# Kernel optimization log

Hardware: AMD Instinct MI355X
Metric: run time of the kernel (lower is better)

The kernel has to match this reference:

```python
import jax, jax.numpy as jnp
import numpy as np

H_DIM = 64      # input_dim of edge_aggregation (== h_dim)
HID = 128       # hidden_size of each per-edge-type agg MLP
T = 5           # edge_types for non-nba dataset
B, E, N = 64, 1024, 512


def setup_inputs() -> dict:
    key = jax.random.key(0)
    ks = jax.random.split(key, 8)
    edge_distribution = jax.random.uniform(ks[0], (B, E, T), dtype=jnp.float32)
    H = jax.random.uniform(ks[1], (B, E, N), dtype=jnp.float32)
    ori = jax.random.normal(ks[2], (B, N, H_DIM), dtype=jnp.float32)
    s1 = 1.0 / np.sqrt(H_DIM)
    s2 = 1.0 / np.sqrt(HID)
    # stacked per-edge-type MLP params: Linear(64->128) -> ReLU -> Linear(128->64)
    W1 = jax.random.uniform(ks[3], (T, H_DIM, HID), minval=-s1, maxval=s1, dtype=jnp.float32)
    b1 = jax.random.uniform(ks[4], (T, HID), minval=-s1, maxval=s1, dtype=jnp.float32)
    W2 = jax.random.uniform(ks[5], (T, HID, H_DIM), minval=-s2, maxval=s2, dtype=jnp.float32)
    b2 = jax.random.uniform(ks[6], (T, H_DIM), minval=-s2, maxval=s2, dtype=jnp.float32)
    return {"edge_distribution": edge_distribution, "H": H, "ori": ori,
            "W1": W1, "b1": b1, "W2": W2, "b2": b2}


def reference(edge_distribution, H, ori, W1, b1, W2, b2):
    # incidence gather: hyperedge features [B, E, D]
    edges = jnp.matmul(H, ori)
    # per-edge-type 2-layer MLP, vectorized over the T edge types
    h = jax.nn.relu(jnp.einsum('bed,tdh->bteh', edges, W1) + b1[None, :, None, :])
    per_type = jnp.einsum('bteh,thd->bted', h, W2) + b2[None, :, None, :]
    # mixture-weighted sum over edge types -> [B, E, D]
    edge_feature = jnp.einsum('bet,bted->bed', edge_distribution, per_type)
    # scatter back through H^T and concat with original node features
    node_agg = jnp.einsum('ben,bed->bnd', H, edge_feature)  # H^T @ edge_feature
    node_feature = jnp.concatenate((node_agg, ori), axis=-1)  # [B, N, 2D]
    return node_feature
```

## Files before the change

kernel.cpp:

```cpp
#include <hip/hip_runtime.h>

#define B_   64
#define E_   1024
#define N_   512
#define D_   64
#define HID_ 128
#define T_   5

typedef __bf16 bf16x8 __attribute__((ext_vector_type(8)));
typedef float f32x4 __attribute__((ext_vector_type(4)));

__device__ __forceinline__ unsigned short f2bu(float f) {
    union { float f; unsigned int u; } v; v.f = f;
    unsigned int r = (v.u + 0x7fffu + ((v.u >> 16) & 1u)) >> 16;
    return (unsigned short)r;
}

__device__ __forceinline__ unsigned int pack2(float lo, float hi) {
    union { __bf16 b[2]; unsigned int u; } v;
    v.b[0] = (__bf16)lo; v.b[1] = (__bf16)hi;
    return v.u;
}

__device__ __forceinline__ uint4 cvt8(float4 a, float4 b) {
    union { __bf16 h[8]; uint4 u; } v;
    v.h[0] = (__bf16)a.x; v.h[1] = (__bf16)a.y; v.h[2] = (__bf16)a.z; v.h[3] = (__bf16)a.w;
    v.h[4] = (__bf16)b.x; v.h[5] = (__bf16)b.y; v.h[6] = (__bf16)b.z; v.h[7] = (__bf16)b.w;
    return v.u;
}

#define MFMA16(a, b, c) __builtin_amdgcn_mfma_f32_16x16x32_bf16((a), (b), (c), 0, 0, 0)

__global__ __launch_bounds__(256) void k_prep_w(const float* __restrict__ W1,
                                                const float* __restrict__ W2,
                                                unsigned short* __restrict__ W1T,
                                                unsigned short* __restrict__ W2T) {
    int idx = blockIdx.x * 256 + threadIdx.x;
    if (idx < T_ * HID_ * D_) {
        int t = idx / (HID_ * D_), rem = idx % (HID_ * D_);
        int h = rem / D_, d = rem % D_;
        W1T[idx] = f2bu(W1[(t * D_ + d) * HID_ + h]);
    } else {
        int j = idx - T_ * HID_ * D_;
        int t = j / (D_ * HID_), rem = j % (D_ * HID_);
        int d = rem / HID_, h = rem % HID_;
        W2T[j] = f2bu(W2[(t * HID_ + h) * D_ + d]);
    }
}

__global__ __launch_bounds__(256) void k_ori_prep(const float* __restrict__ ori,
                                                  float* __restrict__ out,
                                                  unsigned short* __restrict__ oriT) {
    int b = blockIdx.y, n0 = blockIdx.x * 64;
    __shared__ float tl[64 * 65];
    int tid = threadIdx.x;
    int dl = tid & 63;
    #pragma unroll 4
    for (int p = 0; p < 16; ++p) {
        int nn = p * 4 + (tid >> 6);
        float v = ori[(size_t)(b * N_ + n0 + nn) * D_ + dl];
        out[(size_t)(b * N_ + n0 + nn) * 128 + 64 + dl] = v;
        tl[dl * 65 + nn] = v;
    }
    __syncthreads();
    #pragma unroll 4
    for (int p = 0; p < 16; ++p) {
        int dd = p * 4 + (tid >> 6);
        oriT[(size_t)(b * D_ + dd) * N_ + n0 + dl] = f2bu(tl[dd * 65 + dl]);
    }
}

__global__ __launch_bounds__(256, 3) void k_edge_mlp(const float* __restrict__ H,
                                                     const unsigned short* __restrict__ oriT,
                                                     const float* __restrict__ ed,
                                                     const float* __restrict__ b1,
                                                     const float* __restrict__ b2,
                                                     const unsigned short* __restrict__ W1T,
                                                     const unsigned short* __restrict__ W2T,
                                                     unsigned short* __restrict__ efT) {
    int bid = blockIdx.x;
    int bx = (bid & 7) * 128 + (bid >> 3);
    int b = bx >> 4, e0 = (bx & 15) * 64;
    __shared__ __align__(16) unsigned short X[18432];
    __shared__ __align__(16) unsigned short a_sh[64 * 72];
    __shared__ float wd_sh[320];
    __shared__ float b1_sh[640];
    __shared__ float b2_sh[320];
    int tid = threadIdx.x, w = tid >> 6, l = tid & 63, q = l >> 4, c = l & 15;
    int rs = tid >> 3, sgs = tid & 7;

    uint4 w1r[4], w2r[4];
    #pragma unroll
    for (int p = 0; p < 4; ++p) {
        int u2 = p * 256 + tid;
        w1r[p] = *(const uint4*)&W1T[(u2 >> 3) * D_ + (u2 & 7) * 8];
        w2r[p] = *(const uint4*)&W2T[(u2 >> 4) * HID_ + (u2 & 15) * 8];
    }

    for (int u = tid; u < 320; u += 256) wd_sh[u] = ed[((size_t)b * E_ + e0) * T_ + u];
    for (int u = tid; u < 640; u += 256) b1_sh[u] = b1[u];
    for (int u = tid; u < 320; u += 256) b2_sh[u] = b2[u];

    const f32x4 zero = {0.f, 0.f, 0.f, 0.f};

    f32x4 acc1[4];
    #pragma unroll
    for (int fn = 0; fn < 4; ++fn) acc1[fn] = zero;

    const float* Hb = &H[((size_t)b * E_ + e0) * N_];
    const unsigned short* Ob = &oriT[(size_t)b * D_ * N_];

    float4 f00, f01, f10, f11;
    uint4 ob0, ob1;
    {
        const float* s0 = Hb + (size_t)rs * N_ + sgs * 8;
        const float* s1 = Hb + (size_t)(rs + 32) * N_ + sgs * 8;
        f00 = *(const float4*)&s0[0]; f01 = *(const float4*)&s0[4];
        f10 = *(const float4*)&s1[0]; f11 = *(const float4*)&s1[4];
        ob0 = *(const uint4*)&Ob[(size_t)rs * N_ + sgs * 8];
        ob1 = *(const uint4*)&Ob[(size_t)(rs + 32) * N_ + sgs * 8];
    }
    {
        unsigned short* aA = X;
        unsigned short* bB = X + 4608;
        *(uint4*)&aA[rs * 72 + sgs * 8] = cvt8(f00, f01);
        *(uint4*)&aA[(rs + 32) * 72 + sgs * 8] = cvt8(f10, f11);
        *(uint4*)&bB[rs * 72 + sgs * 8] = ob0;
        *(uint4*)&bB[(rs + 32) * 72 + sgs * 8] = ob1;
    }
    __syncthreads();

    for (int ks = 0; ks < 8; ++ks) {
        if (ks < 7) {
            int k0 = (ks + 1) * 64;
            const float* s0 = Hb + (size_t)rs * N_ + k0 + sgs * 8;
            const float* s1 = Hb + (size_t)(rs + 32) * N_ + k0 + sgs * 8;
            f00 = *(const float4*)&s0[0]; f01 = *(const float4*)&s0[4];
            f10 = *(const float4*)&s1[0]; f11 = *(const float4*)&s1[4];
            ob0 = *(const uint4*)&Ob[(size_t)rs * N_ + k0 + sgs * 8];
            ob1 = *(const uint4*)&Ob[(size_t)(rs + 32) * N_ + k0 + sgs * 8];
        }
        const unsigned short* aA = X + (ks & 1) * 9216;
        const unsigned short* bB = aA + 4608;
        #pragma unroll
        for (int hh = 0; hh < 2; ++hh) {
            bf16x8 a0 = *(const bf16x8*)&aA[(w * 16 + c) * 72 + hh * 32 + q * 8];
            #pragma unroll
            for (int fn = 0; fn < 4; ++fn) {
                bf16x8 bb = *(const bf16x8*)&bB[(fn * 16 + c) * 72 + hh * 32 + q * 8];
                acc1[fn] = MFMA16(a0, bb, acc1[fn]);
            }
        }
        if (ks < 7) {
            unsigned short* aN = X + ((ks & 1) ^ 1) * 9216;
            unsigned short* bN = aN + 4608;
            *(uint4*)&aN[rs * 72 + sgs * 8] = cvt8(f00, f01);
            *(uint4*)&aN[(rs + 32) * 72 + sgs * 8] = cvt8(f10, f11);
            *(uint4*)&bN[rs * 72 + sgs * 8] = ob0;
            *(uint4*)&bN[(rs + 32) * 72 + sgs * 8] = ob1;
            __syncthreads();
        }
    }
    #pragma unroll
    for (int fn = 0; fn < 4; ++fn)
        #pragma unroll
        for (int i = 0; i < 4; ++i)
            a_sh[(w * 16 + q * 4 + i) * 72 + fn * 16 + c] = f2bu(acc1[fn][i]);

    f32x4 y[4];
    #pragma unroll
    for (int fn = 0; fn < 4; ++fn) y[fn] = zero;

    unsigned short* w_sh = X;
    unsigned short* h_sh = X + 9216;

    for (int t = 0; t < T_; ++t) {
        __syncthreads();
        #pragma unroll
        for (int p = 0; p < 4; ++p) {
            int u2 = p * 256 + tid;
            *(uint4*)&w_sh[(u2 >> 3) * 72 + (u2 & 7) * 8] = w1r[p];
        }
        if (t < 4) {
            #pragma unroll
            for (int p = 0; p < 4; ++p) {
                int u2 = p * 256 + tid;
                w1r[p] = *(const uint4*)&W1T[((t + 1) * HID_ + (u2 >> 3)) * D_ + (u2 & 7) * 8];
            }
        }
        __syncthreads();
        f32x4 hc[8];
        #pragma unroll
        for (int fn = 0; fn < 8; ++fn) hc[fn] = zero;
        #pragma unroll
        for (int ks = 0; ks < 2; ++ks) {
            bf16x8 a = *(const bf16x8*)&a_sh[(w * 16 + c) * 72 + ks * 32 + q * 8];
            #pragma unroll
            for (int fn = 0; fn < 8; ++fn) {
                bf16x8 bb = *(const bf16x8*)&w_sh[(fn * 16 + c) * 72 + ks * 32 + q * 8];
                hc[fn] = MFMA16(a, bb, hc[fn]);
            }
        }
        float wv[4];
        #pragma unroll
        for (int i = 0; i < 4; ++i) wv[i] = wd_sh[(w * 16 + q * 4 + i) * T_ + t];
        #pragma unroll
        for (int fn = 0; fn < 8; ++fn) {
            float b1v = b1_sh[t * HID_ + fn * 16 + c];
            #pragma unroll
            for (int i = 0; i < 4; ++i) {
                float v = hc[fn][i] + b1v;
                v = fmaxf(v, 0.0f) * wv[i];
                h_sh[(w * 16 + q * 4 + i) * 136 + fn * 16 + c] = f2bu(v);
            }
        }
        __syncthreads();
        #pragma unroll
        for (int p = 0; p < 4; ++p) {
            int u2 = p * 256 + tid;
            *(uint4*)&w_sh[(u2 >> 4) * 136 + (u2 & 15) * 8] = w2r[p];
        }
        if (t < 4) {
            #pragma unroll
            for (int p = 0; p < 4; ++p) {
                int u2 = p * 256 + tid;
                w2r[p] = *(const uint4*)&W2T[((t + 1) * D_ + (u2 >> 4)) * HID_ + (u2 & 15) * 8];
            }
        }
        __syncthreads();
        #pragma unroll
        for (int ks = 0; ks < 4; ++ks) {
            bf16x8 a = *(const bf16x8*)&h_sh[(w * 16 + c) * 136 + ks * 32 + q * 8];
            #pragma unroll
            for (int fn = 0; fn < 4; ++fn) {
                bf16x8 bb = *(const bf16x8*)&w_sh[(fn * 16 + c) * 136 + ks * 32 + q * 8];
                y[fn] = MFMA16(a, bb, y[fn]);
            }
        }
    }
    #pragma unroll
    for (int fn = 0; fn < 4; ++fn) {
        int d = fn * 16 + c;
        ushort4 o;
        #pragma unroll
        for (int i = 0; i < 4; ++i) {
            int r = w * 16 + q * 4 + i;
            float s = y[fn][i];
            #pragma unroll
            for (int t = 0; t < T_; ++t) s += wd_sh[r * T_ + t] * b2_sh[t * D_ + d];
            ((unsigned short*)&o)[i] = f2bu(s);
        }
        *(ushort4*)&efT[((size_t)b * D_ + d) * E_ + e0 + w * 16 + q * 4] = o;
    }
}

__global__ __launch_bounds__(256) void k_gemm_out(const float* __restrict__ H,
                                                  const unsigned short* __restrict__ efT,
                                                  float* __restrict__ out) {
    int bid = blockIdx.x;
    int swz = (bid & 7) * 64 + (bid >> 3);
    int b = swz >> 3, n0 = (swz & 7) * 64;
    __shared__ __align__(16) unsigned short aA[2][64 * 72];
    __shared__ unsigned int bB32[2][64 * 33];
    int tid = threadIdx.x, w = tid >> 6, l = tid & 63, q = l >> 4, c = l & 15;
    int r2 = tid >> 3, cg = tid & 7;
    const f32x4 zero = {0.f, 0.f, 0.f, 0.f};
    f32x4 acc[4];
    #pragma unroll
    for (int fm = 0; fm < 4; ++fm) acc[fm] = zero;

    const unsigned short* Ab = &efT[(size_t)b * D_ * E_];
    const float* Hb = &H[(size_t)b * E_ * N_ + n0];

    uint4 ar0, ar1;
    float4 f0, f1, g0, g1;
    {
        ar0 = *(const uint4*)&Ab[(size_t)r2 * E_ + cg * 8];
        ar1 = *(const uint4*)&Ab[(size_t)(r2 + 32) * E_ + cg * 8];
        const float* s0 = Hb + (size_t)(2 * r2) * N_ + cg * 8;
        const float* s1 = s0 + N_;
        f0 = *(const float4*)&s0[0]; f1 = *(const float4*)&s0[4];
        g0 = *(const float4*)&s1[0]; g1 = *(const float4*)&s1[4];
    }
    {
        *(uint4*)&aA[0][r2 * 72 + cg * 8] = ar0;
        *(uint4*)&aA[0][(r2 + 32) * 72 + cg * 8] = ar1;
        float r0a[8] = {f0.x, f0.y, f0.z, f0.w, f1.x, f1.y, f1.z, f1.w};
        float r1a[8] = {g0.x, g0.y, g0.z, g0.w, g1.x, g1.y, g1.z, g1.w};
        #pragma unroll
        for (int j = 0; j < 8; ++j)
            bB32[0][(cg * 8 + j) * 33 + r2] = pack2(r0a[j], r1a[j]);
    }
    __syncthreads();

    for (int ks = 0; ks < 16; ++ks) {
        if (ks < 15) {
            int k0 = (ks + 1) * 64;
            ar0 = *(const uint4*)&Ab[(size_t)r2 * E_ + k0 + cg * 8];
            ar1 = *(const uint4*)&Ab[(size_t)(r2 + 32) * E_ + k0 + cg * 8];
            const float* s0 = Hb + (size_t)(k0 + 2 * r2) * N_ + cg * 8;
            const float* s1 = s0 + N_;
            f0 = *(const float4*)&s0[0]; f1 = *(const float4*)&s0[4];
            g0 = *(const float4*)&s1[0]; g1 = *(const float4*)&s1[4];
        }
        int cur = ks & 1;
        #pragma unroll
        for (int hh = 0; hh < 2; ++hh) {
            union { unsigned int u[4]; bf16x8 v; } bb;
            #pragma unroll
            for (int i = 0; i < 4; ++i)
                bb.u[i] = bB32[cur][(w * 16 + c) * 33 + hh * 16 + q * 4 + i];
            #pragma unroll
            for (int fm = 0; fm < 4; ++fm) {
                bf16x8 afr = *(const bf16x8*)&aA[cur][(fm * 16 + c) * 72 + hh * 32 + q * 8];
                acc[fm] = MFMA16(afr, bb.v, acc[fm]);
            }
        }
        if (ks < 15) {
            int nxt = cur ^ 1;
            *(uint4*)&aA[nxt][r2 * 72 + cg * 8] = ar0;
            *(uint4*)&aA[nxt][(r2 + 32) * 72 + cg * 8] = ar1;
            float r0a[8] = {f0.x, f0.y, f0.z, f0.w, f1.x, f1.y, f1.z, f1.w};
            float r1a[8] = {g0.x, g0.y, g0.z, g0.w, g1.x, g1.y, g1.z, g1.w};
            #pragma unroll
            for (int j = 0; j < 8; ++j)
                bB32[nxt][(cg * 8 + j) * 33 + r2] = pack2(r0a[j], r1a[j]);
            __syncthreads();
        }
    }
    #pragma unroll
    for (int fm = 0; fm < 4; ++fm) {
        *(f32x4*)&out[((size_t)b * N_ + n0 + w * 16 + c) * 128 + fm * 16 + q * 4] = acc[fm];
    }
}

extern "C" void kernel_launch(void* const* d_in, const int* in_sizes, int n_in,
                              void* d_out, int out_size, void* d_ws, size_t ws_size,
                              hipStream_t stream) {
    const float* ed  = (const float*)d_in[0];
    const float* H   = (const float*)d_in[1];
    const float* ori = (const float*)d_in[2];
    const float* W1  = (const float*)d_in[3];
    const float* b1  = (const float*)d_in[4];
    const float* W2  = (const float*)d_in[5];
    const float* b2  = (const float*)d_in[6];
    float* out = (float*)d_out;

    char* ws = (char*)d_ws;
    unsigned short* oriT = (unsigned short*)ws; ws += (size_t)B_ * D_ * N_ * 2;
    unsigned short* W1T  = (unsigned short*)ws; ws += (size_t)T_ * HID_ * D_ * 2;
    unsigned short* W2T  = (unsigned short*)ws; ws += (size_t)T_ * D_ * HID_ * 2;
    unsigned short* efT  = (unsigned short*)ws; ws += (size_t)B_ * D_ * E_ * 2;

    hipLaunchKernelGGL(k_prep_w, dim3(320), dim3(256), 0, stream, W1, W2, W1T, W2T);
    hipLaunchKernelGGL(k_ori_prep, dim3(8, 64), dim3(256), 0, stream, ori, out, oriT);
    hipLaunchKernelGGL(k_edge_mlp, dim3(1024), dim3(256), 0, stream,
                       H, oriT, ed, b1, b2, W1T, W2T, efT);
    hipLaunchKernelGGL(k_gemm_out, dim3(512), dim3(256), 0, stream, H, efT, out);
}
```

Baseline: 307.7 us.

## Swizzle LDS tiles, read MLP weights from global, drop per-type barriers

Replaces the padded LDS rows (stride 72/136) with XOR-swizzled unpadded rows, which shrinks shared memory. The MLP weight fragments are now read straight from global/L2 instead of being staged through LDS with register prefetch, and the A fragments are hoisted into registers. Each wave keeps its own private h tile, so the per-type __syncthreads calls go away. The occupancy hint (3 blocks) and the blockIdx remapping are also removed. The cost is repeated global loads of the weights on every MFMA and a possible change in L2 locality for H.

After: 336.6 us. 1.09x slower.

```diff
diff --git a/kernel.cpp b/kernel.cpp
--- a/kernel.cpp
+++ b/kernel.cpp
@@ -70,32 +70,23 @@
     }
 }
 
-__global__ __launch_bounds__(256, 3) void k_edge_mlp(const float* __restrict__ H,
-                                                     const unsigned short* __restrict__ oriT,
-                                                     const float* __restrict__ ed,
-                                                     const float* __restrict__ b1,
-                                                     const float* __restrict__ b2,
-                                                     const unsigned short* __restrict__ W1T,
-                                                     const unsigned short* __restrict__ W2T,
-                                                     unsigned short* __restrict__ efT) {
-    int bid = blockIdx.x;
-    int bx = (bid & 7) * 128 + (bid >> 3);
+__global__ __launch_bounds__(256) void k_edge_mlp(const float* __restrict__ H,
+                                                  const unsigned short* __restrict__ oriT,
+                                                  const float* __restrict__ ed,
+                                                  const float* __restrict__ b1,
+                                                  const float* __restrict__ b2,
+                                                  const unsigned short* __restrict__ W1T,
+                                                  const unsigned short* __restrict__ W2T,
+                                                  unsigned short* __restrict__ efT) {
+    int bx = blockIdx.x;
     int b = bx >> 4, e0 = (bx & 15) * 64;
-    __shared__ __align__(16) unsigned short X[18432];
-    __shared__ __align__(16) unsigned short a_sh[64 * 72];
+    __shared__ __align__(16) unsigned short X[16384];
     __shared__ float wd_sh[320];
     __shared__ float b1_sh[640];
     __shared__ float b2_sh[320];
     int tid = threadIdx.x, w = tid >> 6, l = tid & 63, q = l >> 4, c = l & 15;
     int rs = tid >> 3, sgs = tid & 7;
-
-    uint4 w1r[4], w2r[4];
-    #pragma unroll
-    for (int p = 0; p < 4; ++p) {
-        int u2 = p * 256 + tid;
-        w1r[p] = *(const uint4*)&W1T[(u2 >> 3) * D_ + (u2 & 7) * 8];
-        w2r[p] = *(const uint4*)&W2T[(u2 >> 4) * HID_ + (u2 & 15) * 8];
-    }
+    int swsl = (sgs ^ (rs & 7)) * 8;
 
     for (int u = tid; u < 320; u += 256) wd_sh[u] = ed[((size_t)b * E_ + e0) * T_ + u];
     for (int u = tid; u < 640; u += 256) b1_sh[u] = b1[u];
@@ -122,11 +113,11 @@
     }
     {
         unsigned short* aA = X;
-        unsigned short* bB = X + 4608;
-        *(uint4*)&aA[rs * 72 + sgs * 8] = cvt8(f00, f01);
-        *(uint4*)&aA[(rs + 32) * 72 + sgs * 8] = cvt8(f10, f11);
-        *(uint4*)&bB[rs * 72 + sgs * 8] = ob0;
-        *(uint4*)&bB[(rs + 32) * 72 + sgs * 8] = ob1;
+        unsigned short* bB = X + 4096;
+        *(uint4*)&aA[rs * 64 + swsl] = cvt8(f00, f01);
+        *(uint4*)&aA[(rs + 32) * 64 + swsl] = cvt8(f10, f11);
+        *(uint4*)&bB[rs * 64 + swsl] = ob0;
+        *(uint4*)&bB[(rs + 32) * 64 + swsl] = ob1;
     }
     __syncthreads();
 
@@ -140,65 +131,62 @@
             ob0 = *(const uint4*)&Ob[(size_t)rs * N_ + k0 + sgs * 8];
             ob1 = *(const uint4*)&Ob[(size_t)(rs + 32) * N_ + k0 + sgs * 8];
         }
-        const unsigned short* aA = X + (ks & 1) * 9216;
-        const unsigned short* bB = aA + 4608;
+        const unsigned short* aA = X + (ks & 1) * 8192;
+        const unsigned short* bB = aA + 4096;
         #pragma unroll
         for (int hh = 0; hh < 2; ++hh) {
-            bf16x8 a0 = *(const bf16x8*)&aA[(w * 16 + c) * 72 + hh * 32 + q * 8];
+            int sl = ((hh * 4 + q) ^ (c & 7)) * 8;
+            bf16x8 a0 = *(const bf16x8*)&aA[(w * 16 + c) * 64 + sl];
             #pragma unroll
             for (int fn = 0; fn < 4; ++fn) {
-                bf16x8 bb = *(const bf16x8*)&bB[(fn * 16 + c) * 72 + hh * 32 + q * 8];
+                bf16x8 bb = *(const bf16x8*)&bB[(fn * 16 + c) * 64 + sl];
                 acc1[fn] = MFMA16(a0, bb, acc1[fn]);
             }
         }
         if (ks < 7) {
-            unsigned short* aN = X + ((ks & 1) ^ 1) * 9216;
-            unsigned short* bN = aN + 4608;
-            *(uint4*)&aN[rs * 72 + sgs * 8] = cvt8(f00, f01);
-            *(uint4*)&aN[(rs + 32) * 72 + sgs * 8] = cvt8(f10, f11);
-            *(uint4*)&bN[rs * 72 + sgs * 8] = ob0;
-            *(uint4*)&bN[(rs + 32) * 72 + sgs * 8] = ob1;
+            unsigned short* aN = X + ((ks & 1) ^ 1) * 8192;
+            unsigned short* bN = aN + 4096;
+            *(uint4*)&aN[rs * 64 + swsl] = cvt8(f00, f01);
+            *(uint4*)&aN[(rs + 32) * 64 + swsl] = cvt8(f10, f11);
+            *(uint4*)&bN[rs * 64 + swsl] = ob0;
+            *(uint4*)&bN[(rs + 32) * 64 + swsl] = ob1;
             __syncthreads();
         }
     }
+
+    unsigned short* a_sh = X;
     #pragma unroll
     for (int fn = 0; fn < 4; ++fn)
         #pragma unroll
-        for (int i = 0; i < 4; ++i)
-            a_sh[(w * 16 + q * 4 + i) * 72 + fn * 16 + c] = f2bu(acc1[fn][i]);
+        for (int i = 0; i < 4; ++i) {
+            int row = w * 16 + q * 4 + i;
+            a_sh[row * 64 + ((fn * 16 + c) ^ ((row & 7) << 3))] = f2bu(acc1[fn][i]);
+        }
+    __syncthreads();
+
+    bf16x8 afr[2];
+    #pragma unroll
+    for (int ks = 0; ks < 2; ++ks)
+        afr[ks] = *(const bf16x8*)&a_sh[(w * 16 + c) * 64 + ((ks * 32 + q * 8) ^ ((c & 7) << 3))];
+
+    unsigned short* hw = X + 4096 + w * 2048;
 
     f32x4 y[4];
     #pragma unroll
     for (int fn = 0; fn < 4; ++fn) y[fn] = zero;
 
-    unsigned short* w_sh = X;
-    unsigned short* h_sh = X + 9216;
-
     for (int t = 0; t < T_; ++t) {
-        __syncthreads();
-        #pragma unroll
-        for (int p = 0; p < 4; ++p) {
-            int u2 = p * 256 + tid;
-            *(uint4*)&w_sh[(u2 >> 3) * 72 + (u2 & 7) * 8] = w1r[p];
-        }
-        if (t < 4) {
-            #pragma unroll
-            for (int p = 0; p < 4; ++p) {
-                int u2 = p * 256 + tid;
-                w1r[p] = *(const uint4*)&W1T[((t + 1) * HID_ + (u2 >> 3)) * D_ + (u2 & 7) * 8];
-            }
-        }
-        __syncthreads();
+        const unsigned short* W1t = W1T + t * HID_ * D_;
+        const unsigned short* W2t = W2T + t * D_ * HID_;
         f32x4 hc[8];
         #pragma unroll
         for (int fn = 0; fn < 8; ++fn) hc[fn] = zero;
         #pragma unroll
         for (int ks = 0; ks < 2; ++ks) {
-            bf16x8 a = *(const bf16x8*)&a_sh[(w * 16 + c) * 72 + ks * 32 + q * 8];
             #pragma unroll
             for (int fn = 0; fn < 8; ++fn) {
-                bf16x8 bb = *(const bf16x8*)&w_sh[(fn * 16 + c) * 72 + ks * 32 + q * 8];
-                hc[fn] = MFMA16(a, bb, hc[fn]);
+                bf16x8 bb = *(const bf16x8*)&W1t[(fn * 16 + c) * D_ + ks * 32 + q * 8];
+                hc[fn] = MFMA16(afr[ks], bb, hc[fn]);
             }
         }
         float wv[4];
@@ -209,31 +197,17 @@
             float b1v = b1_sh[t * HID_ + fn * 16 + c];
             #pragma unroll
             for (int i = 0; i < 4; ++i) {
-                float v = hc[fn][i] + b1v;
-                v = fmaxf(v, 0.0f) * wv[i];
-                h_sh[(w * 16 + q * 4 + i) * 136 + fn * 16 + c] = f2bu(v);
-            }
-        }
-        __syncthreads();
-        #pragma unroll
-        for (int p = 0; p < 4; ++p) {
-            int u2 = p * 256 + tid;
-            *(uint4*)&w_sh[(u2 >> 4) * 136 + (u2 & 15) * 8] = w2r[p];
-        }
-        if (t < 4) {
-            #pragma unroll
-            for (int p = 0; p < 4; ++p) {
-                int u2 = p * 256 + tid;
-                w2r[p] = *(const uint4*)&W2T[((t + 1) * D_ + (u2 >> 4)) * HID_ + (u2 & 15) * 8];
-            }
-        }
-        __syncthreads();
+                float v = fmaxf(hc[fn][i] + b1v, 0.0f) * wv[i];
+                int row = q * 4 + i;
+                hw[row * 128 + ((fn * 16 + c) ^ ((row & 7) << 3))] = f2bu(v);
+            }
+        }
         #pragma unroll
         for (int ks = 0; ks < 4; ++ks) {
-            bf16x8 a = *(const bf16x8*)&h_sh[(w * 16 + c) * 136 + ks * 32 + q * 8];
+            bf16x8 a = *(const bf16x8*)&hw[c * 128 + ((ks * 32 + q * 8) ^ ((c & 7) << 3))];
             #pragma unroll
             for (int fn = 0; fn < 4; ++fn) {
-                bf16x8 bb = *(const bf16x8*)&w_sh[(fn * 16 + c) * 136 + ks * 32 + q * 8];
+                bf16x8 bb = *(const bf16x8*)&W2t[(fn * 16 + c) * HID_ + ks * 32 + q * 8];
                 y[fn] = MFMA16(a, bb, y[fn]);
             }
         }
```
